# Performance work log

Hardware: AMD Instinct MI355X
Metric: run time of the kernel (lower is better)

Reference implementation:

```python
import jax, jax.numpy as jnp
import numpy as np

B, S, D, H = 2, 2048, 1024, 16
DK = D // H


def setup_inputs() -> dict:
    key = jax.random.key(0)
    ks = jax.random.split(key, 12)
    s = 1.0 / np.sqrt(D)
    inp = {
        "query": jax.random.normal(ks[0], (B, S, D), jnp.float32),
        "key_": jax.random.normal(ks[1], (B, S, D), jnp.float32),
        "value": jax.random.normal(ks[2], (B, S, D), jnp.float32),
        # causal mask, broadcast over heads: [B, 1, S, S]
        "mask": jnp.broadcast_to(jnp.tril(jnp.ones((S, S), bool)), (B, 1, S, S)),
        "W_q": jax.random.uniform(ks[3], (D, D), jnp.float32, -s, s),
        "b_q": jax.random.uniform(ks[4], (D,), jnp.float32, -s, s),
        "W_k": jax.random.uniform(ks[5], (D, D), jnp.float32, -s, s),
        "b_k": jax.random.uniform(ks[6], (D,), jnp.float32, -s, s),
        "W_v": jax.random.uniform(ks[7], (D, D), jnp.float32, -s, s),
        "b_v": jax.random.uniform(ks[8], (D,), jnp.float32, -s, s),
        "W_o": jax.random.uniform(ks[9], (D, D), jnp.float32, -s, s),
        "b_o": jax.random.uniform(ks[10], (D,), jnp.float32, -s, s),
    }
    return inp


def reference(query, key_, value, mask, W_q, b_q, W_k, b_k, W_v, b_v, W_o, b_o):
    b = query.shape[0]
    # linear projections (torch Linear: x @ W.T + b)
    Q = query @ W_q.T + b_q
    K = key_ @ W_k.T + b_k
    V = value @ W_v.T + b_v
    # [b, S, H, dk] -> [b, H, S, dk]
    Q = Q.reshape(b, -1, H, DK).transpose(0, 2, 1, 3)
    K = K.reshape(b, -1, H, DK).transpose(0, 2, 1, 3)
    V = V.reshape(b, -1, H, DK).transpose(0, 2, 1, 3)
    scores = jnp.einsum("bhqd,bhkd->bhqk", Q, K) / jnp.sqrt(jnp.float32(DK))
    scores = jnp.where(mask, scores, -jnp.inf)
    attn = jax.nn.softmax(scores, axis=-1)
    out = jnp.einsum("bhqk,bhkd->bhqd", attn, V)
    out = out.transpose(0, 2, 1, 3).reshape(b, -1, D)
    return out @ W_o.T + b_o
```

## Files before the change

kernel.cpp:

```cpp
#include <hip/hip_runtime.h>
#include <hip/hip_bf16.h>
#include <stdint.h>

#define B_ 2
#define S_ 2048
#define D_ 1024
#define H_ 16
#define DK_ 64

typedef __attribute__((ext_vector_type(4))) float floatx4;
typedef __attribute__((ext_vector_type(8))) short shortx8;
typedef __attribute__((ext_vector_type(4))) short shortx4;
typedef unsigned short ushort_t;

__device__ inline ushort_t f2bf(float f) {
  union { float f; unsigned u; } v; v.f = f;
  unsigned r = v.u + 0x7FFFu + ((v.u >> 16) & 1u);
  return (ushort_t)(r >> 16);
}

__device__ inline unsigned pack2bf(float lo, float hi) {
  return __builtin_amdgcn_perm(__float_as_uint(hi), __float_as_uint(lo), 0x07060302u);
}

__device__ inline shortx4 mk_sx4(unsigned lo, unsigned hi) {
  union { unsigned u[2]; shortx4 s; } v; v.u[0] = lo; v.u[1] = hi; return v.s;
}

__device__ inline shortx8 cat44(shortx4 a, shortx4 b) {
  union { shortx4 s4[2]; shortx8 s8; } v; v.s4[0] = a; v.s4[1] = b; return v.s8;
}

__device__ inline float fast_exp2(float x) {
#if __has_builtin(__builtin_amdgcn_exp2f)
  return __builtin_amdgcn_exp2f(x);
#else
  return __expf(0.69314718056f * x);
#endif
}

__device__ inline void gload_lds16(const void* g, void* l) {
  __builtin_amdgcn_global_load_lds(
      (const __attribute__((address_space(1))) unsigned int*)g,
      (__attribute__((address_space(3))) unsigned int*)l, 16, 0, 0);
}

struct ConvArgs {
  const float* src[7];
  ushort_t* dst[7];
};

__global__ __launch_bounds__(256) void convert_kernel(ConvArgs a) {
  int blk = blockIdx.x;
  int seg, bis;
  if (blk < 3072) { seg = blk >> 10; bis = blk & 1023; }
  else { int bb = blk - 3072; seg = 3 + (bb >> 8); bis = bb & 255; }
  const float4* src = (const float4*)(a.src[seg]) + (size_t)bis * 1024;
  ushort4* dst = (ushort4*)(a.dst[seg]) + (size_t)bis * 1024;
#pragma unroll
  for (int i = 0; i < 4; ++i) {
    int idx = i * 256 + threadIdx.x;
    float4 v = src[idx];
    ushort4 o;
    o.x = f2bf(v.x); o.y = f2bf(v.y); o.z = f2bf(v.z); o.w = f2bf(v.w);
    dst[idx] = o;
  }
}

template <int TM>
__device__ inline void gemm_bk64_core(const ushort_t* __restrict__ A,
                                      const ushort_t* __restrict__ W,
                                      const float* __restrict__ bias,
                                      float scl,
                                      void* __restrict__ outp,
                                      int m0, int n0, int N, int K, int outmode) {
  constexpr int GA = TM / 8;
  constexpr int GB = 16;
  constexpr int GW = (GA + GB) / 4;
  constexpr int MI = TM / 32;
  constexpr int BUFB = (TM + 128) * 128;
  __shared__ uint4 smem4[2 * BUFB / 16];
  char* smem = (char*)&smem4[0];

  const int tid = threadIdx.x;
  const int wave = tid >> 6;
  const int lane = tid & 63;
  const int quad = lane >> 4;
  const int l16 = lane & 15;
  const int wm = (wave >> 1) * (TM / 2);
  const int wn = (wave & 1) * 64;

  floatx4 acc[MI][4] = {};

  const ushort_t* gsrc[GW];
  int ldst[GW];
#pragma unroll
  for (int i = 0; i < GW; ++i) {
    int g = wave * GW + i;
    int r8 = lane >> 3;
    int cs = ((lane & 7) ^ r8) * 8;
    if (g < GA) {
      gsrc[i] = A + (size_t)(m0 + g * 8 + r8) * K + cs;
      ldst[i] = g * 1024 + lane * 16;
    } else {
      gsrc[i] = W + (size_t)(n0 + (g - GA) * 8 + r8) * K + cs;
      ldst[i] = TM * 128 + (g - GA) * 1024 + lane * 16;
    }
  }

#pragma unroll
  for (int i = 0; i < GW; ++i) gload_lds16(gsrc[i], smem + ldst[i]);

  const int niter = K >> 6;
  for (int j = 0; j < niter; ++j) {
    __syncthreads();
    if (j + 1 < niter) {
      const int ko = (j + 1) * 64;
      char* bufn = smem + ((j + 1) & 1) * BUFB;
#pragma unroll
      for (int i = 0; i < GW; ++i) gload_lds16(gsrc[i] + ko, bufn + ldst[i]);
    }
    const char* aT = smem + (j & 1) * BUFB;
    const char* bT = aT + TM * 128;
    shortx8 af[MI][2], bf[4][2];
#pragma unroll
    for (int ks = 0; ks < 2; ++ks) {
      const int co = ((ks * 4 + quad) ^ (l16 & 7)) * 16;
#pragma unroll
      for (int mi = 0; mi < MI; ++mi)
        af[mi][ks] = *(const shortx8*)(aT + (wm + mi * 16 + l16) * 128 + co);
#pragma unroll
      for (int ni = 0; ni < 4; ++ni)
        bf[ni][ks] = *(const shortx8*)(bT + (wn + ni * 16 + l16) * 128 + co);
    }
#pragma unroll
    for (int ks = 0; ks < 2; ++ks)
#pragma unroll
      for (int mi = 0; mi < MI; ++mi)
#pragma unroll
        for (int ni = 0; ni < 4; ++ni)
          acc[mi][ni] = __builtin_amdgcn_mfma_f32_16x16x32_bf16(af[mi][ks], bf[ni][ks], acc[mi][ni], 0, 0, 0);
  }

#pragma unroll
  for (int ni = 0; ni < 4; ++ni) {
    int n = n0 + wn + ni * 16 + l16;
    float bv = bias[n];
#pragma unroll
    for (int mi = 0; mi < MI; ++mi) {
      if (outmode == 2) {
        int m = m0 + wm + mi * 16 + quad * 4;
        int b = m >> 11;
        int s = (m & 2047 & ~31) | (quad * 8 + mi * 4);
        ushort_t* dst = (ushort_t*)outp + (((size_t)(b * 1024 + n)) << 11) + s;
        uint2 pk;
        pk.x = (unsigned)f2bf(acc[mi][ni][0] + bv) |
               ((unsigned)f2bf(acc[mi][ni][1] + bv) << 16);
        pk.y = (unsigned)f2bf(acc[mi][ni][2] + bv) |
               ((unsigned)f2bf(acc[mi][ni][3] + bv) << 16);
        *(uint2*)(dst) = pk;
      } else {
#pragma unroll
        for (int r = 0; r < 4; ++r) {
          int m = m0 + wm + mi * 16 + quad * 4 + r;
          float v = (acc[mi][ni][r] + bv) * scl;
          if (outmode == 1) ((float*)outp)[(size_t)m * N + n] = v;
          else ((ushort_t*)outp)[(size_t)m * N + n] = f2bf(v);
        }
      }
    }
  }
}

struct QkvArgs {
  const ushort_t* A[3];
  const ushort_t* W[3];
  const float* bias[3];
  ushort_t* out[3];
  float scale[3];
};

__global__ __launch_bounds__(256) void gemm_qkv_kernel(QkvArgs a) {
  int z = blockIdx.z;
  int m0 = (blockIdx.x * 8 + (blockIdx.y >> 3)) * 64;
  int n0 = (blockIdx.y & 7) * 128;
  gemm_bk64_core<64>(a.A[z], a.W[z], a.bias[z], a.scale[z], a.out[z],
                     m0, n0, D_, D_, z == 2 ? 2 : 0);
}

__global__ __launch_bounds__(256) void gemm_out_kernel(const ushort_t* __restrict__ A,
                                                       const ushort_t* __restrict__ W,
                                                       const float* __restrict__ bias,
                                                       float* __restrict__ out) {
  int m0 = (blockIdx.x * 8 + (blockIdx.y >> 3)) * 64;
  int n0 = (blockIdx.y & 7) * 128;
  gemm_bk64_core<64>(A, W, bias, 1.0f, out, m0, n0, D_, D_, 1);
}

__global__ __launch_bounds__(256, 2) void attn_kernel(const ushort_t* __restrict__ Qp,
                                                      const ushort_t* __restrict__ Kp,
                                                      const ushort_t* __restrict__ Vt,
                                                      ushort_t* __restrict__ O) {
  const int id = blockIdx.x;
  const int h = id & 15;
  const int u = (id >> 4) & 15;
  const int b = id >> 8;
  const int qt = b ? u : 15 - u;
  const int q0 = qt * 128;
  const int tid = threadIdx.x;
  const int wave = tid >> 6;
  const int lane = tid & 63;
  const int quad = lane >> 4;
  const int l16 = lane & 15;

  __shared__ ushort_t smem[2][8192];

  const size_t hoff = (size_t)h * DK_;

  shortx8 qf[2][2];
#pragma unroll
  for (int grp = 0; grp < 2; ++grp) {
    const ushort_t* qrow = Qp + ((size_t)b * S_ + q0 + wave * 32 + grp * 16 + l16) * D_ + hoff;
    qf[grp][0] = *(const shortx8*)(qrow + quad * 8);
    qf[grp][1] = *(const shortx8*)(qrow + 32 + quad * 8);
  }

  const int r8 = lane >> 3;
  const int cs8 = ((lane & 7) ^ r8) * 8;
  const ushort_t* kb[2];
  const ushort_t* vb[2];
  int kdst[2], vdst[2];
#pragma unroll
  for (int g = 0; g < 2; ++g) {
    const int tr = wave * 16 + g * 8 + r8;
    kb[g] = Kp + ((size_t)b * S_ + tr) * D_ + hoff + cs8;
    vb[g] = Vt + ((size_t)(b * H_ + h) * 64 + tr) * (size_t)S_ + cs8;
    kdst[g] = (wave * 16 + g * 8) * 64 + lane * 8;
    vdst[g] = 4096 + (wave * 16 + g * 8) * 64 + lane * 8;
  }

  floatx4 oacc[2][4] = {};
  float l_run[2] = {0.f, 0.f};
  const int nj = 2 * (qt + 1);
  const int qwave_max = q0 + wave * 32 + 31;

#pragma unroll
  for (int g = 0; g < 2; ++g) {
    gload_lds16(kb[g], &smem[0][kdst[g]]);
    gload_lds16(vb[g], &smem[0][vdst[g]]);
  }

  for (int j = 0; j < nj; ++j) {
    __syncthreads();
    if (j + 1 < nj) {
      ushort_t* bufn = smem[(j + 1) & 1];
      const size_t ko = (size_t)(j + 1) * 64 * D_;
      const int vo = (j + 1) * 64;
#pragma unroll
      for (int g = 0; g < 2; ++g) {
        gload_lds16(kb[g] + ko, bufn + kdst[g]);
        gload_lds16(vb[g] + vo, bufn + vdst[g]);
      }
    }
    const int kbase = j * 64;
    if (kbase > qwave_max) continue;
    const ushort_t* k_lds = smem[j & 1];
    const ushort_t* v_lds = smem[j & 1] + 4096;

    floatx4 sacc[2][4];
    __builtin_amdgcn_s_setprio(1);
#pragma unroll
    for (int kkb = 0; kkb < 4; ++kkb) {
      const ushort_t* krow = k_lds + (kkb * 16 + l16) * 64;
      shortx8 af0 = *(const shortx8*)(krow + (quad ^ (l16 & 7)) * 8);
      shortx8 af1 = *(const shortx8*)(krow + ((4 | quad) ^ (l16 & 7)) * 8);
#pragma unroll
      for (int grp = 0; grp < 2; ++grp) {
        floatx4 acc = {0.f, 0.f, 0.f, 0.f};
        acc = __builtin_amdgcn_mfma_f32_16x16x32_bf16(af0, qf[grp][0], acc, 0, 0, 0);
        acc = __builtin_amdgcn_mfma_f32_16x16x32_bf16(af1, qf[grp][1], acc, 0, 0, 0);
        sacc[grp][kkb] = acc;
      }
    }
    __builtin_amdgcn_s_setprio(0);

#pragma unroll
    for (int grp = 0; grp < 2; ++grp) {
      if (kbase + 63 > q0 + wave * 32 + grp * 16) {
        const int qg = q0 + wave * 32 + grp * 16 + l16;
#pragma unroll
        for (int kkb = 0; kkb < 4; ++kkb)
#pragma unroll
          for (int r = 0; r < 4; ++r)
            if (kbase + kkb * 16 + quad * 4 + r > qg) sacc[grp][kkb][r] = -3.0e38f;
      }
    }

    shortx4 pf[2][4];
#pragma unroll
    for (int grp = 0; grp < 2; ++grp) {
      float psum = 0.f;
#pragma unroll
      for (int kkb = 0; kkb < 4; ++kkb) {
        float p0 = fast_exp2(sacc[grp][kkb][0]);
        float p1 = fast_exp2(sacc[grp][kkb][1]);
        float p2 = fast_exp2(sacc[grp][kkb][2]);
        float p3 = fast_exp2(sacc[grp][kkb][3]);
        psum += (p0 + p1) + (p2 + p3);
        pf[grp][kkb] = mk_sx4(pack2bf(p0, p1), pack2bf(p2, p3));
      }
      l_run[grp] += psum;
    }

    __builtin_amdgcn_s_setprio(1);
#pragma unroll
    for (int kp = 0; kp < 2; ++kp) {
      const shortx8 pf8a = cat44(pf[0][kp * 2], pf[0][kp * 2 + 1]);
      const shortx8 pf8b = cat44(pf[1][kp * 2], pf[1][kp * 2 + 1]);
      const int jj = ((kp * 4 + quad) ^ (l16 & 7)) * 8;
#pragma unroll
      for (int db = 0; db < 4; ++db) {
        const shortx8 vf8 = *(const shortx8*)(v_lds + (db * 16 + l16) * 64 + jj);
        oacc[0][db] = __builtin_amdgcn_mfma_f32_16x16x32_bf16(vf8, pf8a, oacc[0][db], 0, 0, 0);
        oacc[1][db] = __builtin_amdgcn_mfma_f32_16x16x32_bf16(vf8, pf8b, oacc[1][db], 0, 0, 0);
      }
    }
    __builtin_amdgcn_s_setprio(0);
  }

  __syncthreads();
  ushort_t* sm = &smem[0][0];
#pragma unroll
  for (int grp = 0; grp < 2; ++grp) {
    float l0 = l_run[grp];
    l0 += __shfl_xor(l0, 16);
    l0 += __shfl_xor(l0, 32);
    float inv_l = 1.0f / l0;
    int row = wave * 32 + grp * 16 + l16;
#pragma unroll
    for (int db = 0; db < 4; ++db) {
#pragma unroll
      for (int rr = 0; rr < 2; ++rr) {
        unsigned pk = pack2bf(oacc[grp][db][rr * 2] * inv_l, oacc[grp][db][rr * 2 + 1] * inv_l);
        *(unsigned*)(sm + row * 72 + db * 16 + quad * 4 + rr * 2) = pk;
      }
    }
  }
  __syncthreads();
  {
    int r = tid >> 1, c = (tid & 1) * 32;
    const ushort_t* src = sm + r * 72 + c;
    ushort_t* dst = O + ((size_t)b * S_ + q0 + r) * D_ + hoff + c;
    uint4 v0 = *(const uint4*)(src);
    uint4 v1 = *(const uint4*)(src + 8);
    uint4 v2 = *(const uint4*)(src + 16);
    uint4 v3 = *(const uint4*)(src + 24);
    *(uint4*)(dst) = v0;
    *(uint4*)(dst + 8) = v1;
    *(uint4*)(dst + 16) = v2;
    *(uint4*)(dst + 24) = v3;
  }
}

extern "C" void kernel_launch(void* const* d_in, const int* in_sizes, int n_in,
                              void* d_out, int out_size, void* d_ws, size_t ws_size,
                              hipStream_t stream) {
  (void)in_sizes; (void)n_in; (void)out_size; (void)ws_size;
  char* ws = (char*)d_ws;
  ushort_t* xq = (ushort_t*)(ws + 0);
  ushort_t* xk = (ushort_t*)(ws + 8388608);
  ushort_t* xv = (ushort_t*)(ws + 16777216);
  ushort_t* wq = (ushort_t*)(ws + 25165824);
  ushort_t* wk = (ushort_t*)(ws + 27262976);
  ushort_t* wv = (ushort_t*)(ws + 29360128);
  ushort_t* wo = (ushort_t*)(ws + 31457280);
  ushort_t* Qp = (ushort_t*)(ws + 33554432);
  ushort_t* Kp = (ushort_t*)(ws + 41943040);
  ushort_t* Vt = (ushort_t*)(ws + 50331648);
  ushort_t* O = xq;

  ConvArgs ca;
  ca.src[0] = (const float*)d_in[0];  ca.dst[0] = xq;
  ca.src[1] = (const float*)d_in[1];  ca.dst[1] = xk;
  ca.src[2] = (const float*)d_in[2];  ca.dst[2] = xv;
  ca.src[3] = (const float*)d_in[4];  ca.dst[3] = wq;
  ca.src[4] = (const float*)d_in[6];  ca.dst[4] = wk;
  ca.src[5] = (const float*)d_in[8];  ca.dst[5] = wv;
  ca.src[6] = (const float*)d_in[10]; ca.dst[6] = wo;
  convert_kernel<<<dim3(4096), dim3(256), 0, stream>>>(ca);

  QkvArgs qa;
  qa.A[0] = xq; qa.W[0] = wq; qa.bias[0] = (const float*)d_in[5]; qa.out[0] = Qp;
  qa.A[1] = xk; qa.W[1] = wk; qa.bias[1] = (const float*)d_in[7]; qa.out[1] = Kp;
  qa.A[2] = xv; qa.W[2] = wv; qa.bias[2] = (const float*)d_in[9]; qa.out[2] = Vt;
  qa.scale[0] = 0.125f * 1.44269504089f;
  qa.scale[1] = 1.0f;
  qa.scale[2] = 1.0f;
  gemm_qkv_kernel<<<dim3(8, 64, 3), dim3(256), 0, stream>>>(qa);

  attn_kernel<<<dim3(512), dim3(256), 0, stream>>>(Qp, Kp, Vt, O);

  gemm_out_kernel<<<dim3(8, 64, 1), dim3(256), 0, stream>>>(
      O, wo, (const float*)d_in[11], (float*)d_out);
}
```

Before: 218.6 us.

## Use triple-buffered async LDS pipeline for QKV projection GEMM

```diff
diff --git a/kernel.cpp b/kernel.cpp
--- a/kernel.cpp
+++ b/kernel.cpp
@@ -43,6 +43,14 @@
   __builtin_amdgcn_global_load_lds(
       (const __attribute__((address_space(1))) unsigned int*)g,
       (__attribute__((address_space(3))) unsigned int*)l, 16, 0, 0);
+}
+
+__device__ inline void bar() {
+  asm volatile("" ::: "memory");
+  __builtin_amdgcn_sched_barrier(0);
+  __builtin_amdgcn_s_barrier();
+  __builtin_amdgcn_sched_barrier(0);
+  asm volatile("" ::: "memory");
 }
 
 struct ConvArgs {
@@ -172,6 +180,117 @@
   }
 }
 
+__device__ inline void gemm_qkv_tri_core(const ushort_t* __restrict__ A,
+                                         const ushort_t* __restrict__ W,
+                                         const float* __restrict__ bias,
+                                         float scl,
+                                         void* __restrict__ outp,
+                                         int m0, int n0, int outmode) {
+  constexpr int TM = 64;
+  constexpr int GW = 6;
+  constexpr int BUFB = (TM + 128) * 128;
+  __shared__ uint4 smem4[3 * BUFB / 16];
+  char* smem = (char*)&smem4[0];
+
+  const int tid = threadIdx.x;
+  const int wave = tid >> 6;
+  const int lane = tid & 63;
+  const int quad = lane >> 4;
+  const int l16 = lane & 15;
+  const int wm = (wave >> 1) * 32;
+  const int wn = (wave & 1) * 64;
+
+  floatx4 acc[2][4] = {};
+
+  const ushort_t* gsrc[GW];
+  int ldst[GW];
+#pragma unroll
+  for (int i = 0; i < GW; ++i) {
+    int g = wave * GW + i;
+    int r8 = lane >> 3;
+    int cs = ((lane & 7) ^ r8) * 8;
+    if (g < 8) {
+      gsrc[i] = A + (size_t)(m0 + g * 8 + r8) * 1024 + cs;
+      ldst[i] = g * 1024 + lane * 16;
+    } else {
+      gsrc[i] = W + (size_t)(n0 + (g - 8) * 8 + r8) * 1024 + cs;
+      ldst[i] = TM * 128 + (g - 8) * 1024 + lane * 16;
+    }
+  }
+
+#pragma unroll
+  for (int i = 0; i < GW; ++i) gload_lds16(gsrc[i], smem + ldst[i]);
+#pragma unroll
+  for (int i = 0; i < GW; ++i) gload_lds16(gsrc[i] + 64, smem + BUFB + ldst[i]);
+
+  char* pa = smem;
+  char* pb = smem + BUFB;
+  char* pc = smem + 2 * BUFB;
+
+  for (int j = 0; j < 16; ++j) {
+    if (j < 15) asm volatile("s_waitcnt vmcnt(6)" ::: "memory");
+    else        asm volatile("s_waitcnt vmcnt(0)" ::: "memory");
+    bar();
+
+    const char* aT = pa;
+    const char* bT = pa + TM * 128;
+    shortx8 af[2][2], bf[4][2];
+#pragma unroll
+    for (int ks = 0; ks < 2; ++ks) {
+      const int co = ((ks * 4 + quad) ^ (l16 & 7)) * 16;
+#pragma unroll
+      for (int mi = 0; mi < 2; ++mi)
+        af[mi][ks] = *(const shortx8*)(aT + (wm + mi * 16 + l16) * 128 + co);
+#pragma unroll
+      for (int ni = 0; ni < 4; ++ni)
+        bf[ni][ks] = *(const shortx8*)(bT + (wn + ni * 16 + l16) * 128 + co);
+    }
+
+    if (j + 2 < 16) {
+      const int ko = (j + 2) * 64;
+#pragma unroll
+      for (int i = 0; i < GW; ++i) gload_lds16(gsrc[i] + ko, pc + ldst[i]);
+    }
+
+#pragma unroll
+    for (int ks = 0; ks < 2; ++ks)
+#pragma unroll
+      for (int mi = 0; mi < 2; ++mi)
+#pragma unroll
+        for (int ni = 0; ni < 4; ++ni)
+          acc[mi][ni] = __builtin_amdgcn_mfma_f32_16x16x32_bf16(af[mi][ks], bf[ni][ks], acc[mi][ni], 0, 0, 0);
+
+    char* t = pa; pa = pb; pb = pc; pc = t;
+  }
+
+#pragma unroll
+  for (int ni = 0; ni < 4; ++ni) {
+    int n = n0 + wn + ni * 16 + l16;
+    float bv = bias[n];
+#pragma unroll
+    for (int mi = 0; mi < 2; ++mi) {
+      if (outmode == 2) {
+        int m = m0 + wm + mi * 16 + quad * 4;
+        int b = m >> 11;
+        int s = (m & 2047 & ~31) | (quad * 8 + mi * 4);
+        ushort_t* dst = (ushort_t*)outp + (((size_t)(b * 1024 + n)) << 11) + s;
+        uint2 pk;
+        pk.x = (unsigned)f2bf(acc[mi][ni][0] + bv) |
+               ((unsigned)f2bf(acc[mi][ni][1] + bv) << 16);
+        pk.y = (unsigned)f2bf(acc[mi][ni][2] + bv) |
+               ((unsigned)f2bf(acc[mi][ni][3] + bv) << 16);
+        *(uint2*)(dst) = pk;
+      } else {
+#pragma unroll
+        for (int r = 0; r < 4; ++r) {
+          int m = m0 + wm + mi * 16 + quad * 4 + r;
+          ((ushort_t*)outp)[(size_t)m * 1024 + n] = f2bf((acc[mi][ni][r] + bv) * scl);
+        }
+      }
+    }
+  }
+}
+
 struct QkvArgs {
   const ushort_t* A[3];
   const ushort_t* W[3];
@@ -184,8 +303,8 @@
   int z = blockIdx.z;
   int m0 = (blockIdx.x * 8 + (blockIdx.y >> 3)) * 64;
   int n0 = (blockIdx.y & 7) * 128;
-  gemm_bk64_core<64>(a.A[z], a.W[z], a.bias[z], a.scale[z], a.out[z],
-                     m0, n0, D_, D_, z == 2 ? 2 : 0);
+  gemm_qkv_tri_core(a.A[z], a.W[z], a.bias[z], a.scale[z], a.out[z],
+                    m0, n0, z == 2 ? 2 : 0);
 }
 
 __global__ __launch_bounds__(256) void gemm_out_kernel(const ushort_t* __restrict__ A,
```

Measured after the change: 227.1 us. +3.9%, slower.
